# Kernel optimization log

Measured on AMD Instinct MI355X. Metric: run time of the kernel, lower is better.

## Reference

```python
import jax, jax.numpy as jnp
import numpy as np

B, N, DIM_IN, DIM_OUT, EMBED, CHEB_K = 32, 2000, 64, 64, 16, 3


def setup_inputs() -> dict:
    key = jax.random.key(0)
    ks = jax.random.split(key, 6)
    return {
        "x": jax.random.normal(ks[0], (B, N, DIM_IN), dtype=jnp.float32),
        "node_embeddings": jax.random.normal(ks[1], (N, EMBED), dtype=jnp.float32),
        "nodevec1": jax.random.normal(ks[2], (N, EMBED), dtype=jnp.float32),
        "nodevec2": jax.random.normal(ks[3], (EMBED, N), dtype=jnp.float32),
        "weights_pool": jax.random.normal(ks[4], (EMBED, CHEB_K, DIM_IN, DIM_OUT), dtype=jnp.float32) * 0.1,
        "bias_pool": jax.random.normal(ks[5], (EMBED, DIM_OUT), dtype=jnp.float32) * 0.1,
    }


def reference(x, node_embeddings, nodevec1, nodevec2, weights_pool, bias_pool):
    n = node_embeddings.shape[0]
    # adaptive adjacency: softmax(relu(nodevec1 @ nodevec2)) over rows' neighbors
    s = jax.nn.softmax(jax.nn.relu(nodevec1 @ nodevec2), axis=1)  # [N, N]
    # Chebyshev polynomial stack: T0 = I, T1 = S, Tk = 2 S Tk-1 - Tk-2
    support_set = [jnp.eye(n, dtype=x.dtype), s]
    for _ in range(2, CHEB_K):
        support_set.append(2.0 * s @ support_set[-1] - support_set[-2])
    supports = jnp.stack(support_set, axis=0)  # [K, N, N]
    # node-conditioned weights / bias
    weights = jnp.einsum('nd,dkio->nkio', node_embeddings, weights_pool)  # [N, K, I, O]
    bias = node_embeddings @ bias_pool  # [N, O]
    # graph conv: aggregate then per-node combine
    x_g = jnp.einsum('knm,bmc->bnkc', supports, x)  # [B, N, K, I]
    out = jnp.einsum('bnki,nkio->bno', x_g, weights) + bias  # [B, N, O]
    return out
```

## Files before the change

### kernel.cpp

```cpp
#include <hip/hip_runtime.h>

#define N_NODES 2000
#define NP      2048
#define KB      63
#define KB3     66
#define BATCH   32
#define DIM     64
#define EMB     16
#define KI      192
#define WCOLS   12288

typedef __bf16 bf16;
typedef __attribute__((ext_vector_type(8))) __bf16 bf16x8;
typedef __attribute__((ext_vector_type(4))) float  f32x4;

struct alignas(8) bf16x4pk { bf16 v[4]; };

__device__ __forceinline__ void gl_lds16(const bf16* g, bf16* l) {
    __builtin_amdgcn_global_load_lds(
        (__attribute__((address_space(1))) void*)(g),
        (__attribute__((address_space(3))) void*)(l), 16, 0, 0);
}


__global__ __launch_bounds__(256) void adj_softmax_pack(
    const float* __restrict__ nv1, const float* __restrict__ nv2,
    bf16* __restrict__ Sp)
{
    const int row = blockIdx.x;
    const int tid = threadIdx.x;
    const int j0  = tid * 8;
    __shared__ float sa[EMB];
    __shared__ float wred[4];
    __shared__ float bcast;
    if (tid < EMB) sa[tid] = nv1[row * EMB + tid];
    __syncthreads();

    const bool active = (tid < 250);
    float v[8] = {0,0,0,0,0,0,0,0};
    if (active) {
#pragma unroll
        for (int d = 0; d < EMB; ++d) {
            const float sd = sa[d];
            const float4 q0 = *(const float4*)&nv2[d * N_NODES + j0];
            const float4 q1 = *(const float4*)&nv2[d * N_NODES + j0 + 4];
            v[0] += sd * q0.x; v[1] += sd * q0.y; v[2] += sd * q0.z; v[3] += sd * q0.w;
            v[4] += sd * q1.x; v[5] += sd * q1.y; v[6] += sd * q1.z; v[7] += sd * q1.w;
        }
    }
    float lmax = 0.0f;
#pragma unroll
    for (int jj = 0; jj < 8; ++jj) { v[jj] = fmaxf(v[jj], 0.0f); lmax = fmaxf(lmax, v[jj]); }
#pragma unroll
    for (int off = 32; off > 0; off >>= 1)
        lmax = fmaxf(lmax, __shfl_down(lmax, off, 64));
    if ((tid & 63) == 0) wred[tid >> 6] = lmax;
    __syncthreads();
    if (tid == 0) bcast = fmaxf(fmaxf(wred[0], wred[1]), fmaxf(wred[2], wred[3]));
    __syncthreads();
    const float rmax = bcast;

    float lsum = 0.0f;
    if (active) {
#pragma unroll
        for (int jj = 0; jj < 8; ++jj) { v[jj] = __expf(v[jj] - rmax); lsum += v[jj]; }
    }
#pragma unroll
    for (int off = 32; off > 0; off >>= 1)
        lsum += __shfl_down(lsum, off, 64);
    if ((tid & 63) == 0) wred[tid >> 6] = lsum;
    __syncthreads();
    if (tid == 0) bcast = wred[0] + wred[1] + wred[2] + wred[3];
    __syncthreads();
    const float inv = 1.0f / bcast;

    if (tid < 252) {
        bf16x8 pk;
#pragma unroll
        for (int jj = 0; jj < 8; ++jj)
            pk[jj] = (bf16)(active ? v[jj] * inv : 0.0f);
        const int kb = j0 >> 5, q = (j0 >> 3) & 3;
        const int nt = row >> 6, r = row & 63;
        *(bf16x8*)&Sp[((size_t)(kb * 32 + nt) * 256 + q * 64 + r) * 8] = pk;
    }
}

__global__ __launch_bounds__(256) void transpose_pack_x(
    const float* __restrict__ X, bf16* __restrict__ Xtp, bf16* __restrict__ Xbf)
{
    const int b  = blockIdx.y;
    const int m0 = blockIdx.x * 64;
    const int tid = threadIdx.x;
    __shared__ bf16 T[64][72];
#pragma unroll
    for (int i = 0; i < 4; ++i) {
        int idx = i * 256 + tid;
        int r  = idx >> 4;
        int c4 = (idx & 15) * 4;
        int m  = m0 + r;
        float4 v = make_float4(0.f, 0.f, 0.f, 0.f);
        if (m < N_NODES)
            v = *(const float4*)&X[((size_t)b * N_NODES + m) * DIM + c4];
        bf16x4pk pk;
        pk.v[0] = (bf16)v.x; pk.v[1] = (bf16)v.y;
        pk.v[2] = (bf16)v.z; pk.v[3] = (bf16)v.w;
        if (m < N_NODES)
            *(bf16x4pk*)&Xbf[((size_t)b * N_NODES + m) * DIM + c4] = pk;
        T[c4 + 0][r] = pk.v[0];
        T[c4 + 1][r] = pk.v[1];
        T[c4 + 2][r] = pk.v[2];
        T[c4 + 3][r] = pk.v[3];
    }
    __syncthreads();
#pragma unroll
    for (int i = 0; i < 2; ++i) {
        int idx = i * 256 + tid;
        int c   = idx >> 3;
        int mch = idx & 7;
        int kb  = (m0 >> 5) + (mch >> 2);
        if (kb < KB) {
            int q = mch & 3;
            bf16x8 vv = *(const bf16x8*)&T[c][mch * 8];
            *(bf16x8*)&Xtp[((size_t)(b * KB3 + kb) * 256 + q * 64 + c) * 8] = vv;
        }
    }
}

__global__ __launch_bounds__(256, 2) void spmm_pack(
    const bf16* __restrict__ Ap, const bf16* __restrict__ Btp,
    bf16* __restrict__ Ybf, bf16* __restrict__ Ytp, int write_ytp)
{
    const int ntB = blockIdx.x;
    const int b   = blockIdx.y;
    const int n0  = ntB * 128;
    const int tid = threadIdx.x;
    const int lane = tid & 63, wave = tid >> 6;
    const int l15 = lane & 15, quad = lane >> 4;

    __shared__ bf16 As[2][3 * 4096];
    __shared__ bf16 Bs[2][3 * 2048];

    const bf16* aslab = Ap  + (size_t)(ntB * 2) * 2048 + tid * 8;
    const bf16* bslab = Btp + (size_t)(b * KB3) * 2048 + tid * 8;

#define DMA_STAGE(buf, kb0_) {                                        \
        _Pragma("unroll")                                             \
        for (int j = 0; j < 3; ++j) {                                 \
            const bf16* pa = aslab + (size_t)(kb0_ + j) * (32 * 2048);\
            const bf16* pb = bslab + (size_t)(kb0_ + j) * 2048;       \
            gl_lds16(pa,        &As[buf][j * 4096 + tid * 8]);        \
            gl_lds16(pa + 2048, &As[buf][j * 4096 + 2048 + tid * 8]); \
            gl_lds16(pb,        &Bs[buf][j * 2048 + tid * 8]);  } }

    f32x4 acc[2][4] = {};
    const int ga = (wave >> 1) * 256 + quad * 64 + (wave & 1) * 32;
    const int gb = quad * 64;

    DMA_STAGE(0, 0);
#pragma unroll 1
    for (int s = 0; s < 22; ++s) {
        const int cur = s & 1;
        __syncthreads();
        bf16x8 af[3][2], bfr[3][4];
#pragma unroll
        for (int j = 0; j < 3; ++j) {
#pragma unroll
            for (int t = 0; t < 2; ++t)
                af[j][t]  = *(const bf16x8*)&As[cur][j * 4096 + (ga + t * 16 + l15) * 8];
#pragma unroll
            for (int t = 0; t < 4; ++t)
                bfr[j][t] = *(const bf16x8*)&Bs[cur][j * 2048 + (gb + t * 16 + l15) * 8];
        }
        if (s + 1 < 22) DMA_STAGE(cur ^ 1, (s + 1) * 3);
#pragma unroll
        for (int j = 0; j < 3; ++j)
#pragma unroll
            for (int rt = 0; rt < 2; ++rt)
#pragma unroll
                for (int ct = 0; ct < 4; ++ct)
                    acc[rt][ct] = __builtin_amdgcn_mfma_f32_16x16x32_bf16(
                        af[j][rt], bfr[j][ct], acc[rt][ct], 0, 0, 0);
    }
#undef DMA_STAGE

#pragma unroll
    for (int rt = 0; rt < 2; ++rt) {
        const int nbase = n0 + wave * 32 + rt * 16 + quad * 4;
#pragma unroll
        for (int ct = 0; ct < 4; ++ct) {
            const int c = ct * 16 + l15;
#pragma unroll
            for (int r = 0; r < 4; ++r) {
                int n = nbase + r;
                if (n < N_NODES)
                    Ybf[((size_t)b * N_NODES + n) * DIM + c] = (bf16)acc[rt][ct][r];
            }
            if (write_ytp && nbase + 4 <= N_NODES) {
                const int kb2 = nbase >> 5;
                const int kq  = (nbase & 31) >> 3;
                const int j4  = nbase & 7;
                bf16x4pk pk;
                pk.v[0] = (bf16)acc[rt][ct][0];
                pk.v[1] = (bf16)acc[rt][ct][1];
                pk.v[2] = (bf16)acc[rt][ct][2];
                pk.v[3] = (bf16)acc[rt][ct][3];
                *(bf16x4pk*)&Ytp[((size_t)(b * KB3 + kb2) * 256 + kq * 64 + c) * 8 + j4] = pk;
            }
        }
    }
}

#define Z0   (WCOLS * 32)
#define Z1   (Z0 + N_NODES * 32)
#define Z2   (Z1 + 3 * NP * 32)
__global__ __launch_bounds__(256) void prep_small(
    const float* __restrict__ wp, const float* __restrict__ emb,
    bf16* __restrict__ wpT2, bf16* __restrict__ embp, bf16* __restrict__ Sp63)
{
    int idx = blockIdx.x * 256 + threadIdx.x;
    if (idx < Z0) {
        int col = idx >> 5, d = idx & 31;
        int o  = col / KI;
        int kk = col - o * KI;
        int cheb = kk >> 6, i = kk & 63;
        float v = (d < EMB) ? wp[(((d * 3 + cheb) * 64 + i) * 64) + o] : 0.0f;
        wpT2[idx] = (bf16)v;
    } else if (idx < Z1) {
        int j = idx - Z0;
        int n = j >> 5, d = j & 31;
        float v = (d < EMB) ? emb[n * EMB + d] : 0.0f;
        embp[j] = (bf16)v;
    } else if (idx < Z2) {
        Sp63[idx - Z1] = (bf16)0.0f;
    }
}

__global__ __launch_bounds__(256) void prep_W_mfma(
    const bf16* __restrict__ embp, const bf16* __restrict__ wpT2,
    bf16* __restrict__ W)
{
    const int colbase = blockIdx.x * 256;
    const int n0      = blockIdx.y * 16;
    const int tid  = threadIdx.x;
    const int lane = tid & 63, wave = tid >> 6;
    const int l15 = lane & 15, quad = lane >> 4;

    __shared__ bf16 Cs[16][264];

    const bf16x8 af = *(const bf16x8*)&embp[(n0 + l15) * 32 + quad * 8];
    const f32x4 zero = {};
#pragma unroll
    for (int ct = 0; ct < 4; ++ct) {
        const int col = colbase + wave * 64 + ct * 16 + l15;
        bf16x8 bfr = *(const bf16x8*)&wpT2[(size_t)col * 32 + quad * 8];
        f32x4 acc = __builtin_amdgcn_mfma_f32_16x16x32_bf16(af, bfr, zero, 0, 0, 0);
#pragma unroll
        for (int r = 0; r < 4; ++r)
            Cs[quad * 4 + r][wave * 64 + ct * 16 + l15] = (bf16)acc[r];
    }
    __syncthreads();
    {
        const int row = tid >> 4;
        const int c16 = (tid & 15) * 16;
        bf16x8 v0 = *(const bf16x8*)&Cs[row][c16];
        bf16x8 v1 = *(const bf16x8*)&Cs[row][c16 + 8];
        bf16* dst = &W[(size_t)(n0 + row) * WCOLS + colbase + c16];
        *(bf16x8*)dst       = v0;
        *(bf16x8*)(dst + 8) = v1;
    }
}

__global__ __launch_bounds__(256) void combine_node(
    const bf16* __restrict__ xbf, const bf16* __restrict__ y1bf,
    const bf16* __restrict__ y2bf, const float* __restrict__ emb,
    const float* __restrict__ bp, const bf16* __restrict__ W,
    float* __restrict__ out)
{
    const int n   = blockIdx.x;
    const int tid = threadIdx.x;
    const int lane = tid & 63, wave = tid >> 6;
    const int l15 = lane & 15, quad = lane >> 4;

    __shared__ bf16 As[BATCH][200];
    __shared__ bf16 Ws[DIM][200];
    __shared__ float bias_s[DIM];
    __shared__ float emb_s[EMB];

    if (tid < EMB) emb_s[tid] = emb[n * EMB + tid];

    {
        const int b  = tid >> 3;
        const int c8 = (tid & 7) * 8;
        const size_t base = ((size_t)b * N_NODES + n) * DIM + c8;
        bf16x8 vx = *(const bf16x8*)&xbf [base];
        bf16x8 v1 = *(const bf16x8*)&y1bf[base];
        bf16x8 v2 = *(const bf16x8*)&y2bf[base];
        bf16x8 p2;
#pragma unroll
        for (int e = 0; e < 8; ++e)
            p2[e] = (bf16)(2.0f * (float)v2[e] - (float)vx[e]);
        *(bf16x8*)&As[b][c8]       = vx;
        *(bf16x8*)&As[b][64 + c8]  = v1;
        *(bf16x8*)&As[b][128 + c8] = p2;
    }
    {
        const bf16* Wn = W + (size_t)n * WCOLS;
#pragma unroll
        for (int jj = 0; jj < 6; ++jj) {
            int chunk = jj * 256 + tid;
            int o  = chunk / 24;
            int kc = chunk - o * 24;
            bf16x8 v = *(const bf16x8*)&Wn[(size_t)chunk * 8];
            *(bf16x8*)&Ws[o][kc * 8] = v;
        }
    }
    __syncthreads();

    if (tid < DIM) {
        float s = 0.0f;
#pragma unroll
        for (int d = 0; d < EMB; ++d) s += emb_s[d] * bp[d * DIM + tid];
        bias_s[tid] = s;
    }

    bf16x8 af[2][6];
#pragma unroll
    for (int mt = 0; mt < 2; ++mt)
#pragma unroll
        for (int ks = 0; ks < 6; ++ks)
            af[mt][ks] = *(const bf16x8*)&As[mt * 16 + l15][ks * 32 + quad * 8];

    f32x4 acc[2] = {};
#pragma unroll
    for (int ks = 0; ks < 6; ++ks) {
        bf16x8 bfr = *(const bf16x8*)&Ws[wave * 16 + l15][ks * 32 + quad * 8];
        acc[0] = __builtin_amdgcn_mfma_f32_16x16x32_bf16(af[0][ks], bfr, acc[0], 0, 0, 0);
        acc[1] = __builtin_amdgcn_mfma_f32_16x16x32_bf16(af[1][ks], bfr, acc[1], 0, 0, 0);
    }
    __syncthreads();

    const int o = wave * 16 + l15;
    const float bv = bias_s[o];
#pragma unroll
    for (int mt = 0; mt < 2; ++mt)
#pragma unroll
        for (int r = 0; r < 4; ++r) {
            int b = mt * 16 + quad * 4 + r;
            out[((size_t)b * N_NODES + n) * DIM + o] = acc[mt][r] + bv;
        }
}

extern "C" void kernel_launch(void* const* d_in, const int* in_sizes, int n_in,
                              void* d_out, int out_size, void* d_ws, size_t ws_size,
                              hipStream_t stream) {
    const float* x   = (const float*)d_in[0];
    const float* emb = (const float*)d_in[1];
    const float* nv1 = (const float*)d_in[2];
    const float* nv2 = (const float*)d_in[3];
    const float* wp  = (const float*)d_in[4];
    const float* bp  = (const float*)d_in[5];
    float* out = (float*)d_out;

    char* w = (char*)d_ws;
    bf16* Sp   = (bf16*)w;  w += (size_t)KB3 * NP * 32 * 2;
    bf16* xTp  = (bf16*)w;  w += (size_t)BATCH * KB3 * DIM * 32 * 2;
    bf16* y1Tp = (bf16*)w;  w += (size_t)BATCH * KB3 * DIM * 32 * 2;
    bf16* xbf  = (bf16*)w;  w += (size_t)BATCH * N_NODES * DIM * 2;
    bf16* y1bf = (bf16*)w;  w += (size_t)BATCH * N_NODES * DIM * 2;
    bf16* y2bf = (bf16*)w;  w += (size_t)BATCH * N_NODES * DIM * 2;
    bf16* wpT2 = (bf16*)w;  w += (size_t)WCOLS * 32 * 2;
    bf16* embp = (bf16*)w;  w += (size_t)N_NODES * 32 * 2;
    bf16* W    = (bf16*)w;

    adj_softmax_pack<<<N_NODES, 256, 0, stream>>>(nv1, nv2, Sp);
    transpose_pack_x<<<dim3(32, BATCH), 256, 0, stream>>>(x, xTp, xbf);
    prep_small<<<(Z2 + 255) / 256, 256, 0, stream>>>(
        wp, emb, wpT2, embp, Sp + (size_t)63 * NP * 32);
    prep_W_mfma<<<dim3(WCOLS / 256, N_NODES / 16), 256, 0, stream>>>(embp, wpT2, W);
    spmm_pack<<<dim3(16, BATCH), 256, 0, stream>>>(Sp, xTp,  y1bf, y1Tp, 1);
    spmm_pack<<<dim3(16, BATCH), 256, 0, stream>>>(Sp, y1Tp, y2bf, y1Tp, 0);
    combine_node<<<N_NODES, 256, 0, stream>>>(xbf, y1bf, y2bf, emb, bp, W, out);
}
```

Measured before the change: 174.2 us.

## Process two batches per SpMM block with triple-buffered async LDS pipeline

Each spmm_pack block now handles two batch elements, so every adjacency tile loaded into LDS serves both batches and A traffic is halved. The grid shrinks to 16x16 blocks and each wave accumulates a 64x64 tile. The k-loop becomes a three-stage ring of LDS buffers, synchronised with explicit vmcnt waits and raw barriers so DMA runs two stages ahead. Launch bounds drop to one block per SIMD, trading occupancy and block count (256 blocks) for reuse and deeper prefetch. The clamp on the k-block index makes the final prefetches reload valid data rather than read out of bounds.

```diff
diff --git a/kernel.cpp b/kernel.cpp
--- a/kernel.cpp
+++ b/kernel.cpp
@@ -126,66 +126,78 @@
     }
 }
 
-__global__ __launch_bounds__(256, 2) void spmm_pack(
+__global__ __launch_bounds__(256, 1) void spmm_pack(
     const bf16* __restrict__ Ap, const bf16* __restrict__ Btp,
     bf16* __restrict__ Ybf, bf16* __restrict__ Ytp, int write_ytp)
 {
     const int ntB = blockIdx.x;
-    const int b   = blockIdx.y;
-    const int n0  = ntB * 128;
+    const int bt  = blockIdx.y;
     const int tid = threadIdx.x;
     const int lane = tid & 63, wave = tid >> 6;
+    const int wm = wave >> 1, wn = wave & 1;
     const int l15 = lane & 15, quad = lane >> 4;
 
-    __shared__ bf16 As[2][3 * 4096];
-    __shared__ bf16 Bs[2][3 * 2048];
-
-    const bf16* aslab = Ap  + (size_t)(ntB * 2) * 2048 + tid * 8;
-    const bf16* bslab = Btp + (size_t)(b * KB3) * 2048 + tid * 8;
-
-#define DMA_STAGE(buf, kb0_) {                                        \
-        _Pragma("unroll")                                             \
-        for (int j = 0; j < 3; ++j) {                                 \
-            const bf16* pa = aslab + (size_t)(kb0_ + j) * (32 * 2048);\
-            const bf16* pb = bslab + (size_t)(kb0_ + j) * 2048;       \
-            gl_lds16(pa,        &As[buf][j * 4096 + tid * 8]);        \
-            gl_lds16(pa + 2048, &As[buf][j * 4096 + 2048 + tid * 8]); \
-            gl_lds16(pb,        &Bs[buf][j * 2048 + tid * 8]);  } }
-
-    f32x4 acc[2][4] = {};
-    const int ga = (wave >> 1) * 256 + quad * 64 + (wave & 1) * 32;
-    const int gb = quad * 64;
+    __shared__ bf16 sta[3][2][4096];
+    __shared__ bf16 stb[3][2][2][2048];
+
+    const bf16* aslab = Ap  + (size_t)(2 * ntB) * 2048 + tid * 8;
+    const bf16* b0    = Btp + (size_t)((2 * bt + 0) * KB3) * 2048 + tid * 8;
+    const bf16* b1    = Btp + (size_t)((2 * bt + 1) * KB3) * 2048 + tid * 8;
+
+#define DMA_STAGE(st, s_) {                                              \
+        _Pragma("unroll")                                                \
+        for (int j = 0; j < 2; ++j) {                                    \
+            int kbx = (s_) * 2 + j; if (kbx > 65) kbx = 65;              \
+            const bf16* pa = aslab + (size_t)kbx * 65536;                \
+            gl_lds16(pa,        &sta[st][j][tid * 8]);                   \
+            gl_lds16(pa + 2048, &sta[st][j][2048 + tid * 8]);            \
+            gl_lds16(b0 + (size_t)kbx * 2048, &stb[st][j][0][tid * 8]);  \
+            gl_lds16(b1 + (size_t)kbx * 2048, &stb[st][j][1][tid * 8]);  \
+        } }
+
+#define STAGE_COMPUTE(cur, nxt, s_) {                                    \
+        asm volatile("s_waitcnt vmcnt(8)" ::: "memory");                 \
+        asm volatile("s_barrier" ::: "memory");                          \
+        bf16x8 af[2][4], bfr[2][4];                                      \
+        _Pragma("unroll")                                                \
+        for (int j = 0; j < 2; ++j) {                                    \
+            _Pragma("unroll")                                            \
+            for (int t = 0; t < 4; ++t)                                  \
+                af[j][t] = *(const bf16x8*)&sta[cur][j][wm * 2048 + (quad * 64 + t * 16 + l15) * 8]; \
+            _Pragma("unroll")                                            \
+            for (int t = 0; t < 4; ++t)                                  \
+                bfr[j][t] = *(const bf16x8*)&stb[cur][j][wn][(quad * 64 + t * 16 + l15) * 8]; \
+        }                                                                \
+        DMA_STAGE(nxt, (s_) + 2);                                        \
+        _Pragma("unroll")                                                \
+        for (int j = 0; j < 2; ++j)                                      \
+            _Pragma("unroll")                                            \
+            for (int rt = 0; rt < 4; ++rt)                               \
+                _Pragma("unroll")                                        \
+                for (int ct = 0; ct < 4; ++ct)                           \
+                    acc[rt][ct] = __builtin_amdgcn_mfma_f32_16x16x32_bf16( \
+                        af[j][rt], bfr[j][ct], acc[rt][ct], 0, 0, 0);    \
+        }
+
+    f32x4 acc[4][4] = {};
 
     DMA_STAGE(0, 0);
+    DMA_STAGE(1, 1);
+
 #pragma unroll 1
-    for (int s = 0; s < 22; ++s) {
-        const int cur = s & 1;
-        __syncthreads();
-        bf16x8 af[3][2], bfr[3][4];
-#pragma unroll
-        for (int j = 0; j < 3; ++j) {
-#pragma unroll
-            for (int t = 0; t < 2; ++t)
-                af[j][t]  = *(const bf16x8*)&As[cur][j * 4096 + (ga + t * 16 + l15) * 8];
-#pragma unroll
-            for (int t = 0; t < 4; ++t)
-                bfr[j][t] = *(const bf16x8*)&Bs[cur][j * 2048 + (gb + t * 16 + l15) * 8];
-        }
-        if (s + 1 < 22) DMA_STAGE(cur ^ 1, (s + 1) * 3);
-#pragma unroll
-        for (int j = 0; j < 3; ++j)
-#pragma unroll
-            for (int rt = 0; rt < 2; ++rt)
-#pragma unroll
-                for (int ct = 0; ct < 4; ++ct)
-                    acc[rt][ct] = __builtin_amdgcn_mfma_f32_16x16x32_bf16(
-                        af[j][rt], bfr[j][ct], acc[rt][ct], 0, 0, 0);
+    for (int s = 0; s < 33; s += 3) {
+        STAGE_COMPUTE(0, 2, s);
+        STAGE_COMPUTE(1, 0, s + 1);
+        STAGE_COMPUTE(2, 1, s + 2);
     }
 #undef DMA_STAGE
-
-#pragma unroll
-    for (int rt = 0; rt < 2; ++rt) {
-        const int nbase = n0 + wave * 32 + rt * 16 + quad * 4;
+#undef STAGE_COMPUTE
+
+    const int n0 = ntB * 128;
+    const int b  = 2 * bt + wn;
+#pragma unroll
+    for (int rt = 0; rt < 4; ++rt) {
+        const int nbase = n0 + wm * 64 + rt * 16 + quad * 4;
 #pragma unroll
         for (int ct = 0; ct < 4; ++ct) {
             const int c = ct * 16 + l15;
@@ -377,7 +389,7 @@
     prep_small<<<(Z2 + 255) / 256, 256, 0, stream>>>(
         wp, emb, wpT2, embp, Sp + (size_t)63 * NP * 32);
     prep_W_mfma<<<dim3(WCOLS / 256, N_NODES / 16), 256, 0, stream>>>(embp, wpT2, W);
-    spmm_pack<<<dim3(16, BATCH), 256, 0, stream>>>(Sp, xTp,  y1bf, y1Tp, 1);
-    spmm_pack<<<dim3(16, BATCH), 256, 0, stream>>>(Sp, y1Tp, y2bf, y1Tp, 0);
+    spmm_pack<<<dim3(16, 16), 256, 0, stream>>>(Sp, xTp,  y1bf, y1Tp, 1);
+    spmm_pack<<<dim3(16, 16), 256, 0, stream>>>(Sp, y1Tp, y2bf, y1Tp, 0);
     combine_node<<<N_NODES, 256, 0, stream>>>(xbf, y1bf, y2bf, emb, bp, W, out);
 }
```

Measured after the change: 185.8 us. +6.7%, slower.

## Use triple-buffered LDS pipeline with partial vmcnt waits in spmm_pack

Applied to the files above, without the earlier changes.

Replaces the double-buffered loop, which loaded 3 k-blocks per stage and synchronised with __syncthreads, with a 3-stage ring that loads 2 k-blocks per stage. The DMA is issued two stages ahead, and each stage waits with s_waitcnt vmcnt(6) so only the oldest stage's loads must land before the barrier. The goal is to keep more global-to-LDS transfers in flight and hide memory latency behind MFMA work. In exchange it issues redundant clamped loads at the tail (kb clamped to 65) and relies on hand-written waitcnt and barrier asm being correct.

```diff
diff --git a/kernel.cpp b/kernel.cpp
--- a/kernel.cpp
+++ b/kernel.cpp
@@ -137,51 +137,60 @@
     const int lane = tid & 63, wave = tid >> 6;
     const int l15 = lane & 15, quad = lane >> 4;
 
-    __shared__ bf16 As[2][3 * 4096];
-    __shared__ bf16 Bs[2][3 * 2048];
+    __shared__ bf16 As[3][2][4096];
+    __shared__ bf16 Bs[3][2][2048];
 
     const bf16* aslab = Ap  + (size_t)(ntB * 2) * 2048 + tid * 8;
     const bf16* bslab = Btp + (size_t)(b * KB3) * 2048 + tid * 8;
 
-#define DMA_STAGE(buf, kb0_) {                                        \
+#define DMA_STAGE(st, s_) {                                           \
         _Pragma("unroll")                                             \
-        for (int j = 0; j < 3; ++j) {                                 \
-            const bf16* pa = aslab + (size_t)(kb0_ + j) * (32 * 2048);\
-            const bf16* pb = bslab + (size_t)(kb0_ + j) * 2048;       \
-            gl_lds16(pa,        &As[buf][j * 4096 + tid * 8]);        \
-            gl_lds16(pa + 2048, &As[buf][j * 4096 + 2048 + tid * 8]); \
-            gl_lds16(pb,        &Bs[buf][j * 2048 + tid * 8]);  } }
+        for (int j = 0; j < 2; ++j) {                                 \
+            int kbx = (s_) * 2 + j; if (kbx > 65) kbx = 65;           \
+            const bf16* pa = aslab + (size_t)kbx * (32 * 2048);       \
+            const bf16* pb = bslab + (size_t)kbx * 2048;              \
+            gl_lds16(pa,        &As[st][j][tid * 8]);                 \
+            gl_lds16(pa + 2048, &As[st][j][2048 + tid * 8]);          \
+            gl_lds16(pb,        &Bs[st][j][tid * 8]);  } }
 
     f32x4 acc[2][4] = {};
     const int ga = (wave >> 1) * 256 + quad * 64 + (wave & 1) * 32;
     const int gb = quad * 64;
 
+#define STAGE(cur, s_) {                                              \
+        asm volatile("s_waitcnt vmcnt(6)" ::: "memory");              \
+        asm volatile("s_barrier" ::: "memory");                       \
+        bf16x8 af[2][2], bfr[2][4];                                   \
+        _Pragma("unroll")                                             \
+        for (int j = 0; j < 2; ++j) {                                 \
+            _Pragma("unroll")                                         \
+            for (int t = 0; t < 2; ++t)                               \
+                af[j][t] = *(const bf16x8*)&As[cur][j][(ga + t * 16 + l15) * 8]; \
+            _Pragma("unroll")                                         \
+            for (int t = 0; t < 4; ++t)                               \
+                bfr[j][t] = *(const bf16x8*)&Bs[cur][j][(gb + t * 16 + l15) * 8]; \
+        }                                                             \
+        DMA_STAGE((cur + 2) % 3, (s_) + 2);                           \
+        _Pragma("unroll")                                             \
+        for (int j = 0; j < 2; ++j)                                   \
+          _Pragma("unroll")                                           \
+          for (int rt = 0; rt < 2; ++rt)                              \
+            _Pragma("unroll")                                         \
+            for (int ct = 0; ct < 4; ++ct)                            \
+                acc[rt][ct] = __builtin_amdgcn_mfma_f32_16x16x32_bf16(\
+                    af[j][rt], bfr[j][ct], acc[rt][ct], 0, 0, 0);     \
+        }
+
     DMA_STAGE(0, 0);
+    DMA_STAGE(1, 1);
 #pragma unroll 1
-    for (int s = 0; s < 22; ++s) {
-        const int cur = s & 1;
-        __syncthreads();
-        bf16x8 af[3][2], bfr[3][4];
-#pragma unroll
-        for (int j = 0; j < 3; ++j) {
-#pragma unroll
-            for (int t = 0; t < 2; ++t)
-                af[j][t]  = *(const bf16x8*)&As[cur][j * 4096 + (ga + t * 16 + l15) * 8];
-#pragma unroll
-            for (int t = 0; t < 4; ++t)
-                bfr[j][t] = *(const bf16x8*)&Bs[cur][j * 2048 + (gb + t * 16 + l15) * 8];
-        }
-        if (s + 1 < 22) DMA_STAGE(cur ^ 1, (s + 1) * 3);
-#pragma unroll
-        for (int j = 0; j < 3; ++j)
-#pragma unroll
-            for (int rt = 0; rt < 2; ++rt)
-#pragma unroll
-                for (int ct = 0; ct < 4; ++ct)
-                    acc[rt][ct] = __builtin_amdgcn_mfma_f32_16x16x32_bf16(
-                        af[j][rt], bfr[j][ct], acc[rt][ct], 0, 0, 0);
+    for (int s = 0; s < 33; s += 3) {
+        STAGE(0, s);
+        STAGE(1, s + 1);
+        STAGE(2, s + 2);
     }
 #undef DMA_STAGE
+#undef STAGE
 
 #pragma unroll
     for (int rt = 0; rt < 2; ++rt) {
```

Measured after the change: 178.9 us. +2.7%, slower.

## Fuse prep kernels into one launch and swizzle spmm block mapping for L2 locality

Applied to the files above, without the earlier changes.

Merges the adjacency softmax, x transpose/pack and small weight-prep kernels into a single kernel that dispatches on block index, removing two launches and letting their independent work overlap. The spmm grid becomes 1D with a remapping of block index to node tile and batch. This is meant so that blocks likely scheduled on the same XCD share node tiles of the adjacency matrix and reuse them in L2. The fused kernel's shared memory is the union of its branches, which may slightly affect occupancy.

```diff
diff --git a/kernel.cpp b/kernel.cpp
--- a/kernel.cpp
+++ b/kernel.cpp
@@ -23,105 +23,131 @@
 }
 
 
-__global__ __launch_bounds__(256) void adj_softmax_pack(
+#define Z0   (WCOLS * 32)
+#define Z1   (Z0 + N_NODES * 32)
+#define Z2   (Z1 + 3 * NP * 32)
+#define PREP_SM_BLK   2554
+#define PREP_BLOCKS   (N_NODES + 1024 + PREP_SM_BLK)
+
+__global__ __launch_bounds__(256) void prep_fused(
     const float* __restrict__ nv1, const float* __restrict__ nv2,
-    bf16* __restrict__ Sp)
+    bf16* __restrict__ Sp,
+    const float* __restrict__ X, bf16* __restrict__ Xtp, bf16* __restrict__ Xbf,
+    const float* __restrict__ wp, const float* __restrict__ emb,
+    bf16* __restrict__ wpT2, bf16* __restrict__ embp, bf16* __restrict__ Sp63)
 {
-    const int row = blockIdx.x;
+    const int bid = blockIdx.x;
     const int tid = threadIdx.x;
-    const int j0  = tid * 8;
-    __shared__ float sa[EMB];
-    __shared__ float wred[4];
-    __shared__ float bcast;
-    if (tid < EMB) sa[tid] = nv1[row * EMB + tid];
-    __syncthreads();
-
-    const bool active = (tid < 250);
-    float v[8] = {0,0,0,0,0,0,0,0};
-    if (active) {
-#pragma unroll
-        for (int d = 0; d < EMB; ++d) {
-            const float sd = sa[d];
-            const float4 q0 = *(const float4*)&nv2[d * N_NODES + j0];
-            const float4 q1 = *(const float4*)&nv2[d * N_NODES + j0 + 4];
-            v[0] += sd * q0.x; v[1] += sd * q0.y; v[2] += sd * q0.z; v[3] += sd * q0.w;
-            v[4] += sd * q1.x; v[5] += sd * q1.y; v[6] += sd * q1.z; v[7] += sd * q1.w;
-        }
-    }
-    float lmax = 0.0f;
-#pragma unroll
-    for (int jj = 0; jj < 8; ++jj) { v[jj] = fmaxf(v[jj], 0.0f); lmax = fmaxf(lmax, v[jj]); }
-#pragma unroll
-    for (int off = 32; off > 0; off >>= 1)
-        lmax = fmaxf(lmax, __shfl_down(lmax, off, 64));
-    if ((tid & 63) == 0) wred[tid >> 6] = lmax;
-    __syncthreads();
-    if (tid == 0) bcast = fmaxf(fmaxf(wred[0], wred[1]), fmaxf(wred[2], wred[3]));
-    __syncthreads();
-    const float rmax = bcast;
-
-    float lsum = 0.0f;
-    if (active) {
-#pragma unroll
-        for (int jj = 0; jj < 8; ++jj) { v[jj] = __expf(v[jj] - rmax); lsum += v[jj]; }
-    }
-#pragma unroll
-    for (int off = 32; off > 0; off >>= 1)
-        lsum += __shfl_down(lsum, off, 64);
-    if ((tid & 63) == 0) wred[tid >> 6] = lsum;
-    __syncthreads();
-    if (tid == 0) bcast = wred[0] + wred[1] + wred[2] + wred[3];
-    __syncthreads();
-    const float inv = 1.0f / bcast;
-
-    if (tid < 252) {
-        bf16x8 pk;
-#pragma unroll
-        for (int jj = 0; jj < 8; ++jj)
-            pk[jj] = (bf16)(active ? v[jj] * inv : 0.0f);
-        const int kb = j0 >> 5, q = (j0 >> 3) & 3;
-        const int nt = row >> 6, r = row & 63;
-        *(bf16x8*)&Sp[((size_t)(kb * 32 + nt) * 256 + q * 64 + r) * 8] = pk;
-    }
-}
-
-__global__ __launch_bounds__(256) void transpose_pack_x(
-    const float* __restrict__ X, bf16* __restrict__ Xtp, bf16* __restrict__ Xbf)
-{
-    const int b  = blockIdx.y;
-    const int m0 = blockIdx.x * 64;
-    const int tid = threadIdx.x;
-    __shared__ bf16 T[64][72];
-#pragma unroll
-    for (int i = 0; i < 4; ++i) {
-        int idx = i * 256 + tid;
-        int r  = idx >> 4;
-        int c4 = (idx & 15) * 4;
-        int m  = m0 + r;
-        float4 v = make_float4(0.f, 0.f, 0.f, 0.f);
-        if (m < N_NODES)
-            v = *(const float4*)&X[((size_t)b * N_NODES + m) * DIM + c4];
-        bf16x4pk pk;
-        pk.v[0] = (bf16)v.x; pk.v[1] = (bf16)v.y;
-        pk.v[2] = (bf16)v.z; pk.v[3] = (bf16)v.w;
-        if (m < N_NODES)
-            *(bf16x4pk*)&Xbf[((size_t)b * N_NODES + m) * DIM + c4] = pk;
-        T[c4 + 0][r] = pk.v[0];
-        T[c4 + 1][r] = pk.v[1];
-        T[c4 + 2][r] = pk.v[2];
-        T[c4 + 3][r] = pk.v[3];
-    }
-    __syncthreads();
-#pragma unroll
-    for (int i = 0; i < 2; ++i) {
-        int idx = i * 256 + tid;
-        int c   = idx >> 3;
-        int mch = idx & 7;
-        int kb  = (m0 >> 5) + (mch >> 2);
-        if (kb < KB) {
-            int q = mch & 3;
-            bf16x8 vv = *(const bf16x8*)&T[c][mch * 8];
-            *(bf16x8*)&Xtp[((size_t)(b * KB3 + kb) * 256 + q * 64 + c) * 8] = vv;
+
+    if (bid < N_NODES) {
+        const int row = bid;
+        const int j0  = tid * 8;
+        __shared__ float sa[EMB];
+        __shared__ float wred[4];
+        __shared__ float bcast;
+        if (tid < EMB) sa[tid] = nv1[row * EMB + tid];
+        __syncthreads();
+
+        const bool active = (tid < 250);
+        float v[8] = {0,0,0,0,0,0,0,0};
+        if (active) {
+#pragma unroll
+            for (int d = 0; d < EMB; ++d) {
+                const float sd = sa[d];
+                const float4 q0 = *(const float4*)&nv2[d * N_NODES + j0];
+                const float4 q1 = *(const float4*)&nv2[d * N_NODES + j0 + 4];
+                v[0] += sd * q0.x; v[1] += sd * q0.y; v[2] += sd * q0.z; v[3] += sd * q0.w;
+                v[4] += sd * q1.x; v[5] += sd * q1.y; v[6] += sd * q1.z; v[7] += sd * q1.w;
+            }
+        }
+        float lmax = 0.0f;
+#pragma unroll
+        for (int jj = 0; jj < 8; ++jj) { v[jj] = fmaxf(v[jj], 0.0f); lmax = fmaxf(lmax, v[jj]); }
+#pragma unroll
+        for (int off = 32; off > 0; off >>= 1)
+            lmax = fmaxf(lmax, __shfl_down(lmax, off, 64));
+        if ((tid & 63) == 0) wred[tid >> 6] = lmax;
+        __syncthreads();
+        if (tid == 0) bcast = fmaxf(fmaxf(wred[0], wred[1]), fmaxf(wred[2], wred[3]));
+        __syncthreads();
+        const float rmax = bcast;
+
+        float lsum = 0.0f;
+        if (active) {
+#pragma unroll
+            for (int jj = 0; jj < 8; ++jj) { v[jj] = __expf(v[jj] - rmax); lsum += v[jj]; }
+        }
+#pragma unroll
+        for (int off = 32; off > 0; off >>= 1)
+            lsum += __shfl_down(lsum, off, 64);
+        if ((tid & 63) == 0) wred[tid >> 6] = lsum;
+        __syncthreads();
+        if (tid == 0) bcast = wred[0] + wred[1] + wred[2] + wred[3];
+        __syncthreads();
+        const float inv = 1.0f / bcast;
+
+        if (tid < 252) {
+            bf16x8 pk;
+#pragma unroll
+            for (int jj = 0; jj < 8; ++jj)
+                pk[jj] = (bf16)(active ? v[jj] * inv : 0.0f);
+            const int kb = j0 >> 5, q = (j0 >> 3) & 3;
+            const int nt = row >> 6, r = row & 63;
+            *(bf16x8*)&Sp[((size_t)(kb * 32 + nt) * 256 + q * 64 + r) * 8] = pk;
+        }
+    } else if (bid < N_NODES + 1024) {
+        const int t  = bid - N_NODES;
+        const int b  = t >> 5;
+        const int m0 = (t & 31) * 64;
+        __shared__ bf16 T[64][72];
+#pragma unroll
+        for (int i = 0; i < 4; ++i) {
+            int idx = i * 256 + tid;
+            int r  = idx >> 4;
+            int c4 = (idx & 15) * 4;
+            int m  = m0 + r;
+            float4 v = make_float4(0.f, 0.f, 0.f, 0.f);
+            if (m < N_NODES)
+                v = *(const float4*)&X[((size_t)b * N_NODES + m) * DIM + c4];
+            bf16x4pk pk;
+            pk.v[0] = (bf16)v.x; pk.v[1] = (bf16)v.y;
+            pk.v[2] = (bf16)v.z; pk.v[3] = (bf16)v.w;
+            if (m < N_NODES)
+                *(bf16x4pk*)&Xbf[((size_t)b * N_NODES + m) * DIM + c4] = pk;
+            T[c4 + 0][r] = pk.v[0];
+            T[c4 + 1][r] = pk.v[1];
+            T[c4 + 2][r] = pk.v[2];
+            T[c4 + 3][r] = pk.v[3];
+        }
+        __syncthreads();
+#pragma unroll
+        for (int i = 0; i < 2; ++i) {
+            int idx = i * 256 + tid;
+            int c   = idx >> 3;
+            int mch = idx & 7;
+            int kb  = (m0 >> 5) + (mch >> 2);
+            if (kb < KB) {
+                int q = mch & 3;
+                bf16x8 vv = *(const bf16x8*)&T[c][mch * 8];
+                *(bf16x8*)&Xtp[((size_t)(b * KB3 + kb) * 256 + q * 64 + c) * 8] = vv;
+            }
+        }
+    } else {
+        int idx = (bid - N_NODES - 1024) * 256 + tid;
+        if (idx < Z0) {
+            int col = idx >> 5, d = idx & 31;
+            int o  = col / KI;
+            int kk = col - o * KI;
+            int cheb = kk >> 6, i = kk & 63;
+            float v = (d < EMB) ? wp[(((d * 3 + cheb) * 64 + i) * 64) + o] : 0.0f;
+            wpT2[idx] = (bf16)v;
+        } else if (idx < Z1) {
+            int j = idx - Z0;
+            int n = j >> 5, d = j & 31;
+            float v = (d < EMB) ? emb[n * EMB + d] : 0.0f;
+            embp[j] = (bf16)v;
+        } else if (idx < Z2) {
+            Sp63[idx - Z1] = (bf16)0.0f;
         }
     }
 }
@@ -130,8 +156,10 @@
     const bf16* __restrict__ Ap, const bf16* __restrict__ Btp,
     bf16* __restrict__ Ybf, bf16* __restrict__ Ytp, int write_ytp)
 {
-    const int ntB = blockIdx.x;
-    const int b   = blockIdx.y;
+    const int i = blockIdx.x;
+    const int kx = i & 7, j = i >> 3;
+    const int ntB = (j & 7) + 8 * (kx & 1);
+    const int b   = ((j >> 3) << 2) + (kx >> 1);
     const int n0  = ntB * 128;
     const int tid = threadIdx.x;
     const int lane = tid & 63, wave = tid >> 6;
@@ -145,12 +173,12 @@
 
 #define DMA_STAGE(buf, kb0_) {                                        \
         _Pragma("unroll")                                             \
-        for (int j = 0; j < 3; ++j) {                                 \
-            const bf16* pa = aslab + (size_t)(kb0_ + j) * (32 * 2048);\
-            const bf16* pb = bslab + (size_t)(kb0_ + j) * 2048;       \
-            gl_lds16(pa,        &As[buf][j * 4096 + tid * 8]);        \
-            gl_lds16(pa + 2048, &As[buf][j * 4096 + 2048 + tid * 8]); \
-            gl_lds16(pb,        &Bs[buf][j * 2048 + tid * 8]);  } }
+        for (int jj = 0; jj < 3; ++jj) {                              \
+            const bf16* pa = aslab + (size_t)(kb0_ + jj) * (32 * 2048);\
+            const bf16* pb = bslab + (size_t)(kb0_ + jj) * 2048;      \
+            gl_lds16(pa,        &As[buf][jj * 4096 + tid * 8]);       \
+            gl_lds16(pa + 2048, &As[buf][jj * 4096 + 2048 + tid * 8]);\
+            gl_lds16(pb,        &Bs[buf][jj * 2048 + tid * 8]);  } }
 
     f32x4 acc[2][4] = {};
     const int ga = (wave >> 1) * 256 + quad * 64 + (wave & 1) * 32;
@@ -163,23 +191,23 @@
         __syncthreads();
         bf16x8 af[3][2], bfr[3][4];
 #pragma unroll
-        for (int j = 0; j < 3; ++j) {
+        for (int jj = 0; jj < 3; ++jj) {
 #pragma unroll
             for (int t = 0; t < 2; ++t)
-                af[j][t]  = *(const bf16x8*)&As[cur][j * 4096 + (ga + t * 16 + l15) * 8];
+                af[jj][t]  = *(const bf16x8*)&As[cur][jj * 4096 + (ga + t * 16 + l15) * 8];
 #pragma unroll
             for (int t = 0; t < 4; ++t)
-                bfr[j][t] = *(const bf16x8*)&Bs[cur][j * 2048 + (gb + t * 16 + l15) * 8];
+                bfr[jj][t] = *(const bf16x8*)&Bs[cur][jj * 2048 + (gb + t * 16 + l15) * 8];
         }
         if (s + 1 < 22) DMA_STAGE(cur ^ 1, (s + 1) * 3);
 #pragma unroll
-        for (int j = 0; j < 3; ++j)
+        for (int jj = 0; jj < 3; ++jj)
 #pragma unroll
             for (int rt = 0; rt < 2; ++rt)
 #pragma unroll
                 for (int ct = 0; ct < 4; ++ct)
                     acc[rt][ct] = __builtin_amdgcn_mfma_f32_16x16x32_bf16(
-                        af[j][rt], bfr[j][ct], acc[rt][ct], 0, 0, 0);
+                        af[jj][rt], bfr[jj][ct], acc[rt][ct], 0, 0, 0);
     }
 #undef DMA_STAGE
 
@@ -210,31 +238,6 @@
     }
 }
 
-#define Z0   (WCOLS * 32)
-#define Z1   (Z0 + N_NODES * 32)
-#define Z2   (Z1 + 3 * NP * 32)
-__global__ __launch_bounds__(256) void prep_small(
-    const float* __restrict__ wp, const float* __restrict__ emb,
-    bf16* __restrict__ wpT2, bf16* __restrict__ embp, bf16* __restrict__ Sp63)
-{
-    int idx = blockIdx.x * 256 + threadIdx.x;
-    if (idx < Z0) {
-        int col = idx >> 5, d = idx & 31;
-        int o  = col / KI;
-        int kk = col - o * KI;
-        int cheb = kk >> 6, i = kk & 63;
-        float v = (d < EMB) ? wp[(((d * 3 + cheb) * 64 + i) * 64) + o] : 0.0f;
-        wpT2[idx] = (bf16)v;
-    } else if (idx < Z1) {
-        int j = idx - Z0;
-        int n = j >> 5, d = j & 31;
-        float v = (d < EMB) ? emb[n * EMB + d] : 0.0f;
-        embp[j] = (bf16)v;
-    } else if (idx < Z2) {
-        Sp63[idx - Z1] = (bf16)0.0f;
-    }
-}
-
 __global__ __launch_bounds__(256) void prep_W_mfma(
     const bf16* __restrict__ embp, const bf16* __restrict__ wpT2,
     bf16* __restrict__ W)
@@ -372,12 +375,11 @@
     bf16* embp = (bf16*)w;  w += (size_t)N_NODES * 32 * 2;
     bf16* W    = (bf16*)w;
 
-    adj_softmax_pack<<<N_NODES, 256, 0, stream>>>(nv1, nv2, Sp);
-    transpose_pack_x<<<dim3(32, BATCH), 256, 0, stream>>>(x, xTp, xbf);
-    prep_small<<<(Z2 + 255) / 256, 256, 0, stream>>>(
-        wp, emb, wpT2, embp, Sp + (size_t)63 * NP * 32);
+    prep_fused<<<PREP_BLOCKS, 256, 0, stream>>>(
+        nv1, nv2, Sp, x, xTp, xbf, wp, emb, wpT2, embp,
+        Sp + (size_t)63 * NP * 32);
     prep_W_mfma<<<dim3(WCOLS / 256, N_NODES / 16), 256, 0, stream>>>(embp, wpT2, W);
-    spmm_pack<<<dim3(16, BATCH), 256, 0, stream>>>(Sp, xTp,  y1bf, y1Tp, 1);
-    spmm_pack<<<dim3(16, BATCH), 256, 0, stream>>>(Sp, y1Tp, y2bf, y1Tp, 0);
+    spmm_pack<<<512, 256, 0, stream>>>(Sp, xTp,  y1bf, y1Tp, 1);
+    spmm_pack<<<512, 256, 0, stream>>>(Sp, y1Tp, y2bf, y1Tp, 0);
     combine_node<<<N_NODES, 256, 0, stream>>>(xbf, y1bf, y2bf, emb, bp, W, out);
 }
```

After: 170.1 us. -2.4%, faster.
